# Optimization experiments

Measured on AMD Instinct MI355X. Metric: run time of the kernel, lower is better.

The kernel has to match this reference:

```python
import jax, jax.numpy as jnp
import numpy as np

B, N, D = 4, 4096, 2048
E = D // 2  # inter_channels of the non-local block


def setup_inputs() -> dict:
    key = jax.random.key(0)
    ks = jax.random.split(key, 9)
    s_in = 1.0 / np.sqrt(D)   # conv1d(k=1) default init scale, fan_in=D
    s_e = 1.0 / np.sqrt(E)    # W conv: fan_in=E
    return {
        "images_feat": jax.random.normal(ks[0], (B, N, D), jnp.float32),
        "theta_w": jax.random.uniform(ks[1], (E, D), jnp.float32, -s_in, s_in),
        "theta_b": jax.random.uniform(ks[2], (E,), jnp.float32, -s_in, s_in),
        "phi_w": jax.random.uniform(ks[3], (E, D), jnp.float32, -s_in, s_in),
        "phi_b": jax.random.uniform(ks[4], (E,), jnp.float32, -s_in, s_in),
        "g_w": jax.random.uniform(ks[5], (E, D), jnp.float32, -s_in, s_in),
        "g_b": jax.random.uniform(ks[6], (E,), jnp.float32, -s_in, s_in),
        "W_w": jax.random.uniform(ks[7], (D, E), jnp.float32, -s_e, s_e),
        "W_b": jax.random.uniform(ks[8], (D,), jnp.float32, -s_e, s_e),
    }


def reference(images_feat, theta_w, theta_b, phi_w, phi_b, g_w, g_b, W_w, W_b):
    # Original: permute (B,N,D)->(B,D,N), apply 1x1 Conv1d projections (== linear
    # over the channel dim D), theta@phi^T -> softmax -> @g, W conv back, residual,
    # permute back. Expressed directly on (B,N,D).
    x = images_feat
    theta_x = jnp.einsum("bnd,ed->bne", x, theta_w) + theta_b  # (B,N,E)
    phi_x = jnp.einsum("bnd,ed->bne", x, phi_w) + phi_b        # (B,N,E)
    g_x = jnp.einsum("bnd,ed->bne", x, g_w) + g_b              # (B,N,E)
    f = jnp.einsum("bne,bme->bnm", theta_x, phi_x)             # (B,N,N)
    attn = jax.nn.softmax(f, axis=-1)
    y = jnp.einsum("bnm,bme->bne", attn, g_x)                  # (B,N,E)
    z = jnp.einsum("bne,de->bnd", y, W_w) + W_b + x            # residual, (B,N,D)
    return z
```

## Files before the change

### kernel.cpp

```cpp
#include <hip/hip_runtime.h>

typedef short bf16x8 __attribute__((ext_vector_type(8)));
typedef _Float16 f16x8 __attribute__((ext_vector_type(8)));
typedef float f32x4 __attribute__((ext_vector_type(4)));

__device__ __forceinline__ short f2h(float f) {
  _Float16 h = (_Float16)f;
  return __builtin_bit_cast(short, h);
}
__device__ __forceinline__ float h2f(short s) {
  return (float)__builtin_bit_cast(_Float16, s);
}

__device__ __forceinline__ void gload16(const void* g, void* lds) {
  __builtin_amdgcn_global_load_lds(
      (const __attribute__((address_space(1))) unsigned*)g,
      (__attribute__((address_space(3))) unsigned*)lds, 16, 0, 0);
}

template <int NF, int K, int OMODE, int BIAS_MODE, int RES>
__global__ __launch_bounds__(512, 2) void gemmp(
    const short* __restrict__ A, int lda, long sA,
    const short* __restrict__ B, int ldb, long sB,
    void* __restrict__ Cv, int ldc, long sC,
    const float* __restrict__ bias, const float* __restrict__ resid, long sR) {
  constexpr int ACH = 16384;
  constexpr int BCH = NF * 4096;
  constexpr int CH = ACH + BCH;
  constexpr int NP = K / 32;
  __shared__ char lds[4 * CH];

  A += (size_t)blockIdx.z * sA;
  B += (size_t)blockIdx.z * sB;
  char* Cb = (char*)Cv + (size_t)blockIdx.z * sC * (OMODE == 0 ? 4 : 2);
  const float* res = resid ? resid + (size_t)blockIdx.z * sR : nullptr;

  const int tid = threadIdx.x;
  const int wid = tid >> 6, lane = tid & 63;
  const int wr = wid >> 2, wc = wid & 3;
  const int fr = lane & 15, fq = lane >> 4;
  const size_t bm = (size_t)blockIdx.y * 256;
  const size_t bn = (size_t)blockIdx.x * (NF * 64);

  const char* Ag = (const char*)A;
  const char* Bg = (const char*)B;

  const int swz = (fr & 3) << 4;
  int aoff[8], boff[NF];
#pragma unroll
  for (int m = 0; m < 8; m++)
    aoff[m] = (wr * 128 + m * 16 + fr) * 64 + ((fq * 16) ^ swz);
#pragma unroll
  for (int n = 0; n < NF; n++)
    boff[n] = ACH + (wc * NF * 16 + n * 16 + fr) * 64 + ((fq * 16) ^ swz);

  f32x4 acc[8][NF];
#pragma unroll
  for (int m = 0; m < 8; m++)
#pragma unroll
    for (int n = 0; n < NF; n++) acc[m][n] = (f32x4){0.f, 0.f, 0.f, 0.f};

  auto stage = [&](int p) {
    char* s = &lds[(p & 3) * CH];
    const int ktB = p * 64;
#pragma unroll
    for (int i = 0; i < 2; ++i) {
      const int gi = (wid * 2 + i) * 64 + lane;
      const int r = gi >> 2, c = gi & 3;
      gload16(Ag + (size_t)(bm + r) * (size_t)(lda * 2) + ktB +
                  ((c ^ (r & 3)) * 16),
              s + (wid * 2 + i) * 1024);
    }
    if constexpr (NF == 4) {
#pragma unroll
      for (int i = 0; i < 2; ++i) {
        const int gi = (wid * 2 + i) * 64 + lane;
        const int r = gi >> 2, c = gi & 3;
        gload16(Bg + (size_t)(bn + r) * (size_t)(ldb * 2) + ktB +
                    ((c ^ (r & 3)) * 16),
                s + ACH + (wid * 2 + i) * 1024);
      }
    } else {
      const int gi = wid * 64 + lane;
      const int r = gi >> 2, c = gi & 3;
      gload16(Bg + (size_t)(bn + r) * (size_t)(ldb * 2) + ktB +
                  ((c ^ (r & 3)) * 16),
              s + ACH + wid * 1024);
    }
  };

  stage(0);
  stage(1);
#pragma unroll 4
  for (int P = 0; P < NP; ++P) {
    if (P + 2 < NP) stage(P + 2);
    __builtin_amdgcn_sched_barrier(0);
    if (P + 2 < NP) {
      if constexpr (NF == 4) asm volatile("s_waitcnt vmcnt(8)");
      else                   asm volatile("s_waitcnt vmcnt(6)");
    } else if (P + 1 < NP) {
      if constexpr (NF == 4) asm volatile("s_waitcnt vmcnt(4)");
      else                   asm volatile("s_waitcnt vmcnt(3)");
    } else {
      asm volatile("s_waitcnt vmcnt(0)");
    }
    __builtin_amdgcn_sched_barrier(0);
    __builtin_amdgcn_s_barrier();
    __builtin_amdgcn_sched_barrier(0);
    {
      const char* s = &lds[(P & 3) * CH];
      f16x8 ar[8], br[NF];
#pragma unroll
      for (int m = 0; m < 8; m++) ar[m] = *(const f16x8*)(s + aoff[m]);
#pragma unroll
      for (int n = 0; n < NF; n++) br[n] = *(const f16x8*)(s + boff[n]);
      __builtin_amdgcn_s_setprio(1);
#pragma unroll
      for (int m = 0; m < 8; m++)
#pragma unroll
        for (int n = 0; n < NF; n++)
          acc[m][n] = __builtin_amdgcn_mfma_f32_16x16x32_f16(ar[m], br[n],
                                                             acc[m][n], 0, 0, 0);
      __builtin_amdgcn_s_setprio(0);
    }
    __builtin_amdgcn_sched_barrier(0);
  }

#pragma unroll
  for (int m = 0; m < 8; m++) {
    const size_t row0 = bm + wr * 128 + m * 16 + fq * 4;
#pragma unroll
    for (int n = 0; n < NF; n++) {
      const size_t col = bn + wc * NF * 16 + n * 16 + fr;
      float bcol = (BIAS_MODE == 1) ? bias[col] : 0.f;
#pragma unroll
      for (int r = 0; r < 4; r++) {
        float val = acc[m][n][r];
        const size_t row = row0 + r;
        const size_t idx = row * (size_t)ldc + col;
        if (BIAS_MODE == 1) val += bcol;
        if (BIAS_MODE == 2) val += bias[row];
        if (RES) val += res[idx];
        if (OMODE == 0)
          ((float*)Cb)[idx] = val;
        else
          ((short*)Cb)[idx] = f2h(val);
      }
    }
  }
}

__global__ __launch_bounds__(256) void cvt_f32_f16(const float* __restrict__ s,
                                                   short* __restrict__ d, int n) {
  int i = (blockIdx.x * 256 + threadIdx.x) * 8;
  if (i >= n) return;
  const float4 a = *(const float4*)(s + i);
  const float4 b = *(const float4*)(s + i + 4);
  bf16x8 o;
  o[0] = f2h(a.x); o[1] = f2h(a.y); o[2] = f2h(a.z); o[3] = f2h(a.w);
  o[4] = f2h(b.x); o[5] = f2h(b.y); o[6] = f2h(b.z); o[7] = f2h(b.w);
  *(bf16x8*)(d + i) = o;
}

__global__ __launch_bounds__(256) void softmax_rows(short* __restrict__ S) {
  const size_t row = blockIdx.x;
  short* rp = S + row * 4096;
  const int tid = threadIdx.x;
  const int lane = tid & 63, wid = tid >> 6;
  float v[16];
#pragma unroll
  for (int c = 0; c < 2; c++) {
    bf16x8 xv = *(const bf16x8*)(rp + (c * 256 + tid) * 8);
#pragma unroll
    for (int j = 0; j < 8; j++) v[c * 8 + j] = h2f(xv[j]);
  }
  float m = v[0];
#pragma unroll
  for (int i = 1; i < 16; i++) m = fmaxf(m, v[i]);
#pragma unroll
  for (int off = 32; off >= 1; off >>= 1) m = fmaxf(m, __shfl_xor(m, off));
  __shared__ float red[8];
  if (lane == 0) red[wid] = m;
  __syncthreads();
  m = fmaxf(fmaxf(red[0], red[1]), fmaxf(red[2], red[3]));
  float s = 0.f;
#pragma unroll
  for (int i = 0; i < 16; i++) {
    v[i] = __expf(v[i] - m);
    s += v[i];
  }
#pragma unroll
  for (int off = 32; off >= 1; off >>= 1) s += __shfl_xor(s, off);
  if (lane == 0) red[4 + wid] = s;
  __syncthreads();
  s = (red[4] + red[5]) + (red[6] + red[7]);
  const float rs = 1.0f / s;
#pragma unroll
  for (int c = 0; c < 2; c++) {
    bf16x8 o;
#pragma unroll
    for (int j = 0; j < 8; j++) o[j] = f2h(v[c * 8 + j] * rs);
    *(bf16x8*)(rp + (c * 256 + tid) * 8) = o;
  }
}

extern "C" void kernel_launch(void* const* d_in, const int* in_sizes, int n_in,
                              void* d_out, int out_size, void* d_ws,
                              size_t ws_size, hipStream_t stream) {
  const float* x   = (const float*)d_in[0];
  const float* thw = (const float*)d_in[1];
  const float* thb = (const float*)d_in[2];
  const float* phw = (const float*)d_in[3];
  const float* phb = (const float*)d_in[4];
  const float* gw  = (const float*)d_in[5];
  const float* gbi = (const float*)d_in[6];
  const float* Ww  = (const float*)d_in[7];
  const float* Wb  = (const float*)d_in[8];
  float* out = (float*)d_out;

  char* ws = (char*)d_ws;
  short* xf   = (short*)(ws);
  short* wcat = (short*)(ws + 67108864);
  short* gwb  = (short*)(ws + 75497472);
  short* wWb  = (short*)(ws + 79691776);
  float* bc   = (float*)(ws + 83886080);
  short* tpf  = (short*)(ws + 83894272);
  short* gT   = (short*)(ws + 151003136);
  short* sc   = (short*)(ws);

  cvt_f32_f16<<<16384, 256, 0, stream>>>(x, xf, 33554432);
  cvt_f32_f16<<<1024, 256, 0, stream>>>(thw, wcat, 2097152);
  cvt_f32_f16<<<1024, 256, 0, stream>>>(phw, wcat + 2097152, 2097152);
  cvt_f32_f16<<<1024, 256, 0, stream>>>(gw, gwb, 2097152);
  cvt_f32_f16<<<1024, 256, 0, stream>>>(Ww, wWb, 2097152);
  hipMemcpyAsync(bc, thb, 4096, hipMemcpyDeviceToDevice, stream);
  hipMemcpyAsync(bc + 1024, phb, 4096, hipMemcpyDeviceToDevice, stream);

  gemmp<4, 2048, 1, 1, 0><<<dim3(8, 64, 1), 512, 0, stream>>>(
      xf, 2048, 0L, wcat, 2048, 0L, tpf, 2048, 0L, bc, nullptr, 0L);

  gemmp<4, 2048, 1, 2, 0><<<dim3(16, 4, 4), 512, 0, stream>>>(
      gwb, 2048, 0L, xf, 2048, 8388608L, gT, 4096, 4194304L, gbi, nullptr, 0L);

  for (int p = 0; p < 2; ++p) {
    const short* tp = tpf + (size_t)p * 16777216;
    gemmp<4, 1024, 1, 0, 0><<<dim3(16, 16, 2), 512, 0, stream>>>(
        tp, 2048, 8388608L, tp + 1024, 2048, 8388608L,
        sc, 4096, 16777216L, nullptr, nullptr, 0L);
    softmax_rows<<<8192, 256, 0, stream>>>(sc);
    short* yp = tpf + (size_t)p * 16777216;
    gemmp<2, 4096, 1, 0, 0><<<dim3(8, 16, 2), 512, 0, stream>>>(
        sc, 4096, 16777216L, gT + (size_t)p * 8388608, 4096, 4194304L,
        yp, 1024, 4194304L, nullptr, nullptr, 0L);
    gemmp<4, 1024, 0, 1, 1><<<dim3(8, 16, 2), 512, 0, stream>>>(
        yp, 1024, 4194304L, wWb, 1024, 0L,
        out + (size_t)p * 16777216, 2048, 8388608L,
        Wb, x + (size_t)p * 16777216, 8388608L);
  }
}
```

Baseline: 762.7 us.

## Double-buffer LDS fragment reads in GEMM and precompute swizzled load offsets

Restructures the GEMM main loop so fragments for the next k-step are read from LDS into a second register set while MFMAs run on the current set. It also replaces the per-stage address arithmetic with precomputed offsets and adopts a new XOR swizzle, applied consistently to global_load_lds writes and fragment reads, to cut LDS bank conflicts. The aim is to hide LDS read latency behind the MFMAs and reduce address VALU work. In exchange it roughly doubles fragment register pressure under the 512x2 launch bound, and the unrolled loop assumes NP is even.

After: 755.2 us. No clear change (-1.0%).

```diff
diff --git a/kernel.cpp b/kernel.cpp
--- a/kernel.cpp
+++ b/kernel.cpp
@@ -16,6 +16,11 @@
   __builtin_amdgcn_global_load_lds(
       (const __attribute__((address_space(1))) unsigned*)g,
       (__attribute__((address_space(3))) unsigned*)lds, 16, 0, 0);
+}
+
+__device__ __forceinline__ int swzF(int a) { return a ^ ((a >> 2) & 0x70); }
+__device__ __forceinline__ int swzI(int s) {
+  return s ^ ((((s >> 2) ^ (s >> 4)) & 0x10) | ((s >> 2) & 0x60));
 }
 
 template <int NF, int K, int OMODE, int BIAS_MODE, int RES>
@@ -28,7 +33,7 @@
   constexpr int BCH = NF * 4096;
   constexpr int CH = ACH + BCH;
   constexpr int NP = K / 32;
-  __shared__ char lds[4 * CH];
+  __shared__ __align__(1024) char lds[4 * CH];
 
   A += (size_t)blockIdx.z * sA;
   B += (size_t)blockIdx.z * sB;
@@ -44,15 +49,35 @@
 
   const char* Ag = (const char*)A;
   const char* Bg = (const char*)B;
-
-  const int swz = (fr & 3) << 4;
-  int aoff[8], boff[NF];
-#pragma unroll
-  for (int m = 0; m < 8; m++)
-    aoff[m] = (wr * 128 + m * 16 + fr) * 64 + ((fq * 16) ^ swz);
-#pragma unroll
-  for (int n = 0; n < NF; n++)
-    boff[n] = ACH + (wc * NF * 16 + n * 16 + fr) * 64 + ((fq * 16) ^ swz);
+  const int ldaB = lda * 2, ldbB = ldb * 2;
+
+  int offA[2], offB[2], dstA[2], dstB[2];
+#pragma unroll
+  for (int i = 0; i < 2; ++i) {
+    const int d = ((wid * 2 + i) * 64 + lane) * 16;
+    const int a = swzI(d);
+    offA[i] = (int)(bm * 0) + (a >> 6) * ldaB + (a & 63);
+    dstA[i] = (wid * 2 + i) * 1024;
+  }
+  const size_t Abase = bm * (size_t)ldaB;
+  size_t Bbase = bn * (size_t)ldbB;
+  if constexpr (NF == 4) {
+#pragma unroll
+    for (int i = 0; i < 2; ++i) {
+      const int d = ((wid * 2 + i) * 64 + lane) * 16;
+      const int a = swzI(d);
+      offB[i] = (a >> 6) * ldbB + (a & 63);
+      dstB[i] = ACH + (wid * 2 + i) * 1024;
+    }
+  } else {
+    const int d = (wid * 64 + lane) * 16;
+    const int a = swzI(d);
+    offB[0] = (a >> 6) * ldbB + (a & 63);
+    dstB[0] = ACH + wid * 1024;
+  }
+
+  const int aoff0 = swzF((wr * 128 + fr) * 64 + fq * 16);
+  const int boff0 = ACH + swzF((wc * NF * 16 + fr) * 64 + fq * 16);
 
   f32x4 acc[8][NF];
 #pragma unroll
@@ -63,68 +88,91 @@
   auto stage = [&](int p) {
     char* s = &lds[(p & 3) * CH];
     const int ktB = p * 64;
-#pragma unroll
-    for (int i = 0; i < 2; ++i) {
-      const int gi = (wid * 2 + i) * 64 + lane;
-      const int r = gi >> 2, c = gi & 3;
-      gload16(Ag + (size_t)(bm + r) * (size_t)(lda * 2) + ktB +
-                  ((c ^ (r & 3)) * 16),
-              s + (wid * 2 + i) * 1024);
-    }
-    if constexpr (NF == 4) {
-#pragma unroll
-      for (int i = 0; i < 2; ++i) {
-        const int gi = (wid * 2 + i) * 64 + lane;
-        const int r = gi >> 2, c = gi & 3;
-        gload16(Bg + (size_t)(bn + r) * (size_t)(ldb * 2) + ktB +
-                    ((c ^ (r & 3)) * 16),
-                s + ACH + (wid * 2 + i) * 1024);
-      }
-    } else {
-      const int gi = wid * 64 + lane;
-      const int r = gi >> 2, c = gi & 3;
-      gload16(Bg + (size_t)(bn + r) * (size_t)(ldb * 2) + ktB +
-                  ((c ^ (r & 3)) * 16),
-              s + ACH + wid * 1024);
-    }
+    gload16(Ag + Abase + (size_t)(offA[0] + ktB), s + dstA[0]);
+    gload16(Ag + Abase + (size_t)(offA[1] + ktB), s + dstA[1]);
+    gload16(Bg + Bbase + (size_t)(offB[0] + ktB), s + dstB[0]);
+    if constexpr (NF == 4)
+      gload16(Bg + Bbase + (size_t)(offB[1] + ktB), s + dstB[1]);
   };
+
+  f16x8 a0[8], b0[NF], a1[8], b1[NF];
 
   stage(0);
   stage(1);
-#pragma unroll 4
-  for (int P = 0; P < NP; ++P) {
-    if (P + 2 < NP) stage(P + 2);
-    __builtin_amdgcn_sched_barrier(0);
-    if (P + 2 < NP) {
-      if constexpr (NF == 4) asm volatile("s_waitcnt vmcnt(8)");
-      else                   asm volatile("s_waitcnt vmcnt(6)");
-    } else if (P + 1 < NP) {
-      if constexpr (NF == 4) asm volatile("s_waitcnt vmcnt(4)");
-      else                   asm volatile("s_waitcnt vmcnt(3)");
-    } else {
-      asm volatile("s_waitcnt vmcnt(0)");
-    }
-    __builtin_amdgcn_sched_barrier(0);
-    __builtin_amdgcn_s_barrier();
-    __builtin_amdgcn_sched_barrier(0);
-    {
-      const char* s = &lds[(P & 3) * CH];
-      f16x8 ar[8], br[NF];
-#pragma unroll
-      for (int m = 0; m < 8; m++) ar[m] = *(const f16x8*)(s + aoff[m]);
-#pragma unroll
-      for (int n = 0; n < NF; n++) br[n] = *(const f16x8*)(s + boff[n]);
-      __builtin_amdgcn_s_setprio(1);
-#pragma unroll
-      for (int m = 0; m < 8; m++)
-#pragma unroll
-        for (int n = 0; n < NF; n++)
-          acc[m][n] = __builtin_amdgcn_mfma_f32_16x16x32_f16(ar[m], br[n],
-                                                             acc[m][n], 0, 0, 0);
-      __builtin_amdgcn_s_setprio(0);
-    }
-    __builtin_amdgcn_sched_barrier(0);
-  }
+  __builtin_amdgcn_sched_barrier(0);
+  if constexpr (NF == 4) { asm volatile("s_waitcnt vmcnt(4)"); }
+  else                   { asm volatile("s_waitcnt vmcnt(3)"); }
+  __builtin_amdgcn_sched_barrier(0);
+  __builtin_amdgcn_s_barrier();
+  __builtin_amdgcn_sched_barrier(0);
+  {
+    const char* s0 = &lds[0];
+#pragma unroll
+    for (int m = 0; m < 8; m++)
+      a0[m] = *(const f16x8*)(s0 + aoff0 + m * 1024);
+#pragma unroll
+    for (int n = 0; n < NF; n++)
+      b0[n] = *(const f16x8*)(s0 + boff0 + n * 1024);
+  }
+
+#define STEADY_PHASE(P, CA, CB, NA, NB)                                      \
+  do {                                                                       \
+    stage((P) + 2);                                                          \
+    __builtin_amdgcn_sched_barrier(0);                                       \
+    if constexpr (NF == 4) { asm volatile("s_waitcnt vmcnt(4)"); }           \
+    else                   { asm volatile("s_waitcnt vmcnt(3)"); }           \
+    __builtin_amdgcn_sched_barrier(0);                                       \
+    __builtin_amdgcn_s_barrier();                                            \
+    __builtin_amdgcn_sched_barrier(0);                                       \
+    {                                                                        \
+      const char* sn = &lds[(((P) + 1) & 3) * CH];                           \
+      _Pragma("unroll") for (int m = 0; m < 8; m++)                          \
+          NA[m] = *(const f16x8*)(sn + aoff0 + m * 1024);                    \
+      _Pragma("unroll") for (int n = 0; n < NF; n++)                         \
+          NB[n] = *(const f16x8*)(sn + boff0 + n * 1024);                    \
+    }                                                                        \
+    __builtin_amdgcn_s_setprio(1);                                           \
+    _Pragma("unroll") for (int m = 0; m < 8; m++)                            \
+      _Pragma("unroll") for (int n = 0; n < NF; n++)                         \
+        acc[m][n] = __builtin_amdgcn_mfma_f32_16x16x32_f16(                  \
+            CA[m], CB[n], acc[m][n], 0, 0, 0);                               \
+    __builtin_amdgcn_s_setprio(0);                                           \
+    __builtin_amdgcn_sched_barrier(0);                                       \
+  } while (0)
+
+  for (int P = 0; P < NP - 2; P += 2) {
+    STEADY_PHASE(P, a0, b0, a1, b1);
+    STEADY_PHASE(P + 1, a1, b1, a0, b0);
+  }
+#undef STEADY_PHASE
+
+  asm volatile("s_waitcnt vmcnt(0)");
+  __builtin_amdgcn_sched_barrier(0);
+  __builtin_amdgcn_s_barrier();
+  __builtin_amdgcn_sched_barrier(0);
+  {
+    const char* sn = &lds[((NP - 1) & 3) * CH];
+#pragma unroll
+    for (int m = 0; m < 8; m++)
+      a1[m] = *(const f16x8*)(sn + aoff0 + m * 1024);
+#pragma unroll
+    for (int n = 0; n < NF; n++)
+      b1[n] = *(const f16x8*)(sn + boff0 + n * 1024);
+  }
+  __builtin_amdgcn_s_setprio(1);
+#pragma unroll
+  for (int m = 0; m < 8; m++)
+#pragma unroll
+    for (int n = 0; n < NF; n++)
+      acc[m][n] = __builtin_amdgcn_mfma_f32_16x16x32_f16(a0[m], b0[n],
+                                                         acc[m][n], 0, 0, 0);
+#pragma unroll
+  for (int m = 0; m < 8; m++)
+#pragma unroll
+    for (int n = 0; n < NF; n++)
+      acc[m][n] = __builtin_amdgcn_mfma_f32_16x16x32_f16(a1[m], b1[n],
+                                                         acc[m][n], 0, 0, 0);
+  __builtin_amdgcn_s_setprio(0);
 
 #pragma unroll
   for (int m = 0; m < 8; m++) {
```
